# Performance work log

Measured on AMD Instinct MI355X. Metric: run time of the kernel, lower is better.

## Reference

```python
import jax, jax.numpy as jnp
import numpy as np

N = 100000   # nodes
E = 1600000  # edges
C = 128      # hidden_channels
L = 3        # num_layers
V = 128      # embedding vocab


def setup_inputs() -> dict:
    key = jax.random.key(0)
    ks = jax.random.split(key, 10)
    s = 1.0 / np.sqrt(C)
    return {
        "x_idx": jax.random.randint(ks[0], (N,), 0, V),
        "edge_index": jax.random.randint(ks[1], (2, E), 0, N),
        "edge_weight": jax.random.uniform(ks[2], (E,), dtype=jnp.float32),
        "emb": jax.random.normal(ks[3], (V, C), dtype=jnp.float32),
        "conv_w": jax.random.uniform(ks[4], (L, C, C), minval=-s, maxval=s, dtype=jnp.float32),
        "conv_b": jnp.zeros((L, C), dtype=jnp.float32),
        "lin1_w": jax.random.uniform(ks[5], (C, C), minval=-s, maxval=s, dtype=jnp.float32),
        "lin1_b": jnp.zeros((C,), dtype=jnp.float32),
        "lin2_w": jax.random.uniform(ks[6], (C, 2), minval=-s, maxval=s, dtype=jnp.float32),
        "lin2_b": jnp.zeros((2,), dtype=jnp.float32),
    }


def reference(x_idx, edge_index, edge_weight, emb, conv_w, conv_b,
              lin1_w, lin1_b, lin2_w, lin2_b):
    # GCNConv (PyG): add self-loops (weight 1), symmetric normalization
    row, col = edge_index[0], edge_index[1]
    loop = jnp.arange(N)
    r = jnp.concatenate([row, loop])
    c = jnp.concatenate([col, loop])
    w = jnp.concatenate([edge_weight, jnp.ones((N,), edge_weight.dtype)])
    deg = jax.ops.segment_sum(w, c, num_segments=N)            # [N]
    dinv = jnp.where(deg > 0, jax.lax.rsqrt(deg), 0.0)
    norm = dinv[r] * w * dinv[c]                               # [E+N]

    x = emb[x_idx]                                             # [N, C]
    for i in range(L):
        xw = x @ conv_w[i]                                     # [N, C]
        # message: norm * xw[src], aggregate at dst
        x = jax.ops.segment_sum(norm[:, None] * xw[r], c, num_segments=N) + conv_b[i]
        if i < L - 1:
            x = jax.nn.relu(x)  # dropout is identity in eval mode

    x = jax.nn.relu(x @ lin1_w + lin1_b)
    return x @ lin2_w + lin2_b                                 # [N, 2]
```

## Files before the change

### kernel.cpp

```cpp
#include <hip/hip_runtime.h>
#include <hip/hip_fp16.h>

#define NN 100000
#define NE 1600000
#define CC 128
#define NB_SCAN 391

typedef _Float16 f16x8 __attribute__((ext_vector_type(8)));
typedef float    f32x4 __attribute__((ext_vector_type(4)));

__global__ void k_init(int* cnt) {
    int i = blockIdx.x * 256 + threadIdx.x;
    if (i < NN) cnt[i] = 0;
}

__global__ void k_count(const int* __restrict__ ei, int* cnt, int* loc) {
    int e = blockIdx.x * 256 + threadIdx.x;
    if (e < NE) {
        int c = ei[NE + e];
        loc[e] = atomicAdd(&cnt[c], 1);
    }
}

__global__ void k_scan1(const int* __restrict__ cnt, int* rowptr, int* bsum) {
    __shared__ int s[256];
    int t = threadIdx.x;
    int i = blockIdx.x * 256 + t;
    int v = (i < NN) ? cnt[i] : 0;
    s[t] = v; __syncthreads();
    for (int off = 1; off < 256; off <<= 1) {
        int x = (t >= off) ? s[t - off] : 0;
        __syncthreads();
        s[t] += x;
        __syncthreads();
    }
    if (i < NN) rowptr[i] = s[t] - v;
    if (t == 255) bsum[blockIdx.x] = s[255];
}

__global__ void k_scan2(const int* __restrict__ bsum, int* boff) {
    __shared__ int s[512];
    int t = threadIdx.x;
    int v = (t < NB_SCAN) ? bsum[t] : 0;
    s[t] = v; __syncthreads();
    for (int off = 1; off < 512; off <<= 1) {
        int x = (t >= off) ? s[t - off] : 0;
        __syncthreads();
        s[t] += x;
        __syncthreads();
    }
    if (t < NB_SCAN) boff[t] = s[t] - v;
}

__global__ void k_scan3(int* rowptr, const int* __restrict__ boff) {
    int i = blockIdx.x * 256 + threadIdx.x;
    if (i < NN) rowptr[i] += boff[i >> 8];
    if (i == 0) rowptr[NN] = NE;
}

__global__ void k_scatter(const int* __restrict__ ei, const float* __restrict__ ew,
                          const int* __restrict__ loc, const int* __restrict__ rowptr,
                          int2* __restrict__ csr) {
    int e = blockIdx.x * 256 + threadIdx.x;
    if (e < NE) {
        int c = ei[NE + e];
        int pos = rowptr[c] + loc[e];
        csr[pos] = make_int2(ei[e], __float_as_int(ew[e]));
    }
}

__global__ void k_degdinv(const int* __restrict__ rowptr, const int2* __restrict__ csr,
                          float* __restrict__ dinv) {
    int v = blockIdx.x * 256 + threadIdx.x;
    if (v < NN) {
        int b = rowptr[v], e = rowptr[v + 1];
        float s = 1.f;
        for (int i = b; i < e; i++) s += __int_as_float(csr[i].y);
        dinv[v] = rsqrtf(s);
    }
}

__global__ void k_mkcsr0(const int2* __restrict__ csr, const int* __restrict__ xidx,
                         const float* __restrict__ dinv, int2* __restrict__ csr0) {
    int e = blockIdx.x * 256 + threadIdx.x;
    if (e < NE) {
        int2 c = csr[e];
        csr0[e] = make_int2(xidx[c.x],
                            __float_as_int(__int_as_float(c.y) * dinv[c.x]));
    }
}

__global__ void k_wcvt(const float* __restrict__ conv_w, const float* __restrict__ lin1_w,
                       _Float16* __restrict__ wt) {
    int t = blockIdx.x * 256 + threadIdx.x;
    int l = t >> 14, r = t & 16383;
    int j = r >> 7, k = r & 127;
    const float* src = (l < 2) ? (conv_w + (l + 1) * 16384) : lin1_w;
    wt[l * 16384 + j * 128 + k] = (_Float16)src[k * 128 + j];
}

__global__ void k_embw(const float* __restrict__ emb, const float* __restrict__ w0,
                       __half2* __restrict__ ewh) {
    int t = blockIdx.x * 256 + threadIdx.x;
    int i = t >> 6, jp = t & 63;
    int j0 = jp * 2;
    float a0 = 0.f, a1 = 0.f;
    for (int k = 0; k < 128; k++) {
        float e = emb[i * 128 + k];
        a0 = fmaf(e, w0[k * 128 + j0], a0);
        a1 = fmaf(e, w0[k * 128 + j0 + 1], a1);
    }
    ewh[t] = __floats2half2_rn(a0, a1);
}

__global__ void k_agg0(const int2* __restrict__ csr0, const int* __restrict__ rowptr,
                       const int* __restrict__ xidx, const float* __restrict__ dinv,
                       const __half2* __restrict__ ewh, const float* __restrict__ bias,
                       __half2* __restrict__ xout) {
    int wave = threadIdx.x >> 6, lane = threadIdx.x & 63;
    int v = blockIdx.x * 4 + wave;
    if (v >= NN) return;
    int beg = rowptr[v], end = rowptr[v + 1];
    float ax = 0.f, ay = 0.f;
    int e = beg;
    while (e + 8 <= end) {
        int2 c[8]; __half2 t[8];
#pragma unroll
        for (int u = 0; u < 8; u++) c[u] = csr0[e + u];
#pragma unroll
        for (int u = 0; u < 8; u++) t[u] = ewh[c[u].x * 64 + lane];
#pragma unroll
        for (int u = 0; u < 8; u++) {
            float w = __int_as_float(c[u].y);
            float2 f = __half22float2(t[u]);
            ax = fmaf(w, f.x, ax);
            ay = fmaf(w, f.y, ay);
        }
        e += 8;
    }
    if (e + 4 <= end) {
        int2 c[4]; __half2 t[4];
#pragma unroll
        for (int u = 0; u < 4; u++) c[u] = csr0[e + u];
#pragma unroll
        for (int u = 0; u < 4; u++) t[u] = ewh[c[u].x * 64 + lane];
#pragma unroll
        for (int u = 0; u < 4; u++) {
            float w = __int_as_float(c[u].y);
            float2 f = __half22float2(t[u]);
            ax = fmaf(w, f.x, ax);
            ay = fmaf(w, f.y, ay);
        }
        e += 4;
    }
    for (; e < end; ++e) {
        int2 c = csr0[e];
        float w = __int_as_float(c.y);
        float2 f = __half22float2(ewh[c.x * 64 + lane]);
        ax = fmaf(w, f.x, ax);
        ay = fmaf(w, f.y, ay);
    }
    float dv = dinv[v];
    float2 ts = __half22float2(ewh[xidx[v] * 64 + lane]);
    ax = fmaf(dv, ts.x, ax);
    ay = fmaf(dv, ts.y, ay);
    float2 b = reinterpret_cast<const float2*>(bias)[lane];
    float ox = fmaxf(fmaf(dv, ax, b.x), 0.f);
    float oy = fmaxf(fmaf(dv, ay, b.y), 0.f);
    xout[v * 64 + lane] = __floats2half2_rn(ox, oy);
}

__global__ void k_agg(const __half2* __restrict__ y2, const int* __restrict__ rowptr,
                      const int2* __restrict__ csr, const float* __restrict__ dinv,
                      const float* __restrict__ bias, __half2* __restrict__ xout,
                      int relu) {
    int wave = threadIdx.x >> 6, lane = threadIdx.x & 63;
    int v = blockIdx.x * 4 + wave;
    if (v >= NN) return;
    int beg = rowptr[v], end = rowptr[v + 1];
    float ax = 0.f, ay = 0.f;
    int e = beg;
    while (e + 8 <= end) {
        int2 c[8]; __half2 t[8];
#pragma unroll
        for (int u = 0; u < 8; u++) c[u] = csr[e + u];
#pragma unroll
        for (int u = 0; u < 8; u++) t[u] = y2[c[u].x * 64 + lane];
#pragma unroll
        for (int u = 0; u < 8; u++) {
            float w = __int_as_float(c[u].y);
            float2 f = __half22float2(t[u]);
            ax = fmaf(w, f.x, ax);
            ay = fmaf(w, f.y, ay);
        }
        e += 8;
    }
    if (e + 4 <= end) {
        int2 c[4]; __half2 t[4];
#pragma unroll
        for (int u = 0; u < 4; u++) c[u] = csr[e + u];
#pragma unroll
        for (int u = 0; u < 4; u++) t[u] = y2[c[u].x * 64 + lane];
#pragma unroll
        for (int u = 0; u < 4; u++) {
            float w = __int_as_float(c[u].y);
            float2 f = __half22float2(t[u]);
            ax = fmaf(w, f.x, ax);
            ay = fmaf(w, f.y, ay);
        }
        e += 4;
    }
    for (; e < end; ++e) {
        int2 c = csr[e];
        float w = __int_as_float(c.y);
        float2 f = __half22float2(y2[c.x * 64 + lane]);
        ax = fmaf(w, f.x, ax);
        ay = fmaf(w, f.y, ay);
    }
    float2 self = __half22float2(y2[v * 64 + lane]);
    ax += self.x; ay += self.y;
    float s = dinv[v];
    float2 b = reinterpret_cast<const float2*>(bias)[lane];
    float ox = fmaf(s, ax, b.x);
    float oy = fmaf(s, ay, b.y);
    if (relu) { ox = fmaxf(ox, 0.f); oy = fmaxf(oy, 0.f); }
    xout[v * 64 + lane] = __floats2half2_rn(ox, oy);
}

template <int MODE>
__global__ __launch_bounds__(256) void k_mgemm(const _Float16* __restrict__ A,
                                               const _Float16* __restrict__ Wt,
                                               const float* __restrict__ dinv,
                                               const float* __restrict__ bias,
                                               _Float16* __restrict__ yout,
                                               const float* __restrict__ w2,
                                               const float* __restrict__ b2,
                                               float* __restrict__ outf) {
    int wid = threadIdx.x >> 6, lane = threadIdx.x & 63;
    int lc = lane & 15, lg = lane >> 4;
    int arow = blockIdx.x * 64 + wid * 16 + lc;
    bool rok = arow < NN;

    f32x4 acc[8];
#pragma unroll
    for (int j = 0; j < 8; j++) acc[j] = (f32x4){0.f, 0.f, 0.f, 0.f};

#pragma unroll
    for (int kc = 0; kc < 4; kc++) {
        int k0 = kc * 32 + lg * 8;
        f16x8 a = {0, 0, 0, 0, 0, 0, 0, 0};
        if (rok) a = *reinterpret_cast<const f16x8*>(&A[arow * 128 + k0]);
#pragma unroll
        for (int j = 0; j < 8; j++) {
            f16x8 b = *reinterpret_cast<const f16x8*>(&Wt[(j * 16 + lc) * 128 + k0]);
            acc[j] = __builtin_amdgcn_mfma_f32_16x16x32_f16(a, b, acc[j], 0, 0, 0);
        }
    }

    int orow0 = blockIdx.x * 64 + wid * 16 + lg * 4;
    if (MODE == 0) {
        float dv[4];
#pragma unroll
        for (int r = 0; r < 4; r++)
            dv[r] = (orow0 + r < NN) ? dinv[orow0 + r] : 0.f;
#pragma unroll
        for (int j = 0; j < 8; j++) {
#pragma unroll
            for (int r = 0; r < 4; r++) {
                int orow = orow0 + r;
                if (orow < NN)
                    yout[orow * 128 + j * 16 + lc] = (_Float16)(dv[r] * acc[j][r]);
            }
        }
    } else {
        float bj[8], w0j[8], w1j[8];
#pragma unroll
        for (int j = 0; j < 8; j++) {
            int c = j * 16 + lc;
            bj[j] = bias[c];
            w0j[j] = w2[c * 2 + 0];
            w1j[j] = w2[c * 2 + 1];
        }
        float bb0 = b2[0], bb1 = b2[1];
#pragma unroll
        for (int r = 0; r < 4; r++) {
            float p0 = 0.f, p1 = 0.f;
#pragma unroll
            for (int j = 0; j < 8; j++) {
                float h = fmaxf(acc[j][r] + bj[j], 0.f);
                p0 = fmaf(h, w0j[j], p0);
                p1 = fmaf(h, w1j[j], p1);
            }
#pragma unroll
            for (int m = 1; m < 16; m <<= 1) {
                p0 += __shfl_xor(p0, m);
                p1 += __shfl_xor(p1, m);
            }
            int orow = orow0 + r;
            if (lc == 0 && orow < NN)
                *reinterpret_cast<float2*>(&outf[orow * 2]) =
                    make_float2(p0 + bb0, p1 + bb1);
        }
    }
}

extern "C" void kernel_launch(void* const* d_in, const int* in_sizes, int n_in,
                              void* d_out, int out_size, void* d_ws, size_t ws_size,
                              hipStream_t stream) {
    const int*   x_idx  = (const int*)d_in[0];
    const int*   ei     = (const int*)d_in[1];
    const float* ew     = (const float*)d_in[2];
    const float* emb    = (const float*)d_in[3];
    const float* conv_w = (const float*)d_in[4];
    const float* conv_b = (const float*)d_in[5];
    const float* lin1_w = (const float*)d_in[6];
    const float* lin1_b = (const float*)d_in[7];
    const float* lin2_w = (const float*)d_in[8];
    const float* lin2_b = (const float*)d_in[9];
    float* out = (float*)d_out;

    char* ws = (char*)d_ws;
    size_t off = 0;
    auto alloc = [&](size_t bytes) -> void* {
        void* p = ws + off;
        off += (bytes + 255) & ~(size_t)255;
        return p;
    };
    float*    dinv   = (float*)alloc(NN * 4);
    int*      cnt    = (int*)alloc(NN * 4);
    int*      rowptr = (int*)alloc((NN + 1) * 4);
    int*      bsum   = (int*)alloc(512 * 4);
    int*      boff   = (int*)alloc(512 * 4);
    int*      loc    = (int*)alloc((size_t)NE * 4);
    int2*     csr    = (int2*)alloc((size_t)NE * 8);
    int2*     csr0   = (int2*)alloc((size_t)NE * 8);
    __half2*  ewh    = (__half2*)alloc(128 * 64 * 4);
    _Float16* wt     = (_Float16*)alloc(3 * 128 * 128 * 2);
    __half*   xbuf   = (__half*)alloc((size_t)NN * CC * 2);
    __half*   ybuf   = (__half*)alloc((size_t)NN * CC * 2);
    (void)ws_size;

    const int NBn = (NN + 255) / 256;
    const int NBe = (NE + 255) / 256;
    const int NBg = (NN + 63) / 64;

    k_init<<<NBn, 256, 0, stream>>>(cnt);
    k_count<<<NBe, 256, 0, stream>>>(ei, cnt, loc);
    k_scan1<<<NB_SCAN, 256, 0, stream>>>(cnt, rowptr, bsum);
    k_scan2<<<1, 512, 0, stream>>>(bsum, boff);
    k_scan3<<<NBn, 256, 0, stream>>>(rowptr, boff);
    k_scatter<<<NBe, 256, 0, stream>>>(ei, ew, loc, rowptr, csr);
    k_degdinv<<<NBn, 256, 0, stream>>>(rowptr, csr, dinv);
    k_mkcsr0<<<NBe, 256, 0, stream>>>(csr, x_idx, dinv, csr0);
    k_wcvt<<<192, 256, 0, stream>>>(conv_w, lin1_w, wt);

    k_embw<<<32, 256, 0, stream>>>(emb, conv_w, ewh);
    k_agg0<<<NN / 4, 256, 0, stream>>>(csr0, rowptr, x_idx, dinv, ewh,
                                       conv_b + 0 * CC, (__half2*)xbuf);
    k_mgemm<0><<<NBg, 256, 0, stream>>>((const _Float16*)xbuf, wt + 0 * 16384, dinv,
                                        nullptr, (_Float16*)ybuf, nullptr, nullptr,
                                        nullptr);
    k_agg<<<NN / 4, 256, 0, stream>>>((const __half2*)ybuf, rowptr, csr, dinv,
                                      conv_b + 1 * CC, (__half2*)xbuf, 1);
    k_mgemm<0><<<NBg, 256, 0, stream>>>((const _Float16*)xbuf, wt + 1 * 16384, dinv,
                                        nullptr, (_Float16*)ybuf, nullptr, nullptr,
                                        nullptr);
    k_agg<<<NN / 4, 256, 0, stream>>>((const __half2*)ybuf, rowptr, csr, dinv,
                                      conv_b + 2 * CC, (__half2*)xbuf, 0);
    k_mgemm<1><<<NBg, 256, 0, stream>>>((const _Float16*)xbuf, wt + 2 * 16384, dinv,
                                        lin1_b, nullptr, lin2_w, lin2_b, out);
}
```

Baseline: 444.6 us.

## Pad CSR rows to multiples of 4 and gather 4 edges per wave

Each node's CSR segment is padded to a multiple of 4 edges, with zero-weight padding entries that come from a memset of a larger buffer. The aggregation kernels split each wave into 4 groups of 16 lanes, so one wave loads 4 neighbor rows at a time with 16-byte f16x8 loads, then combines the partial sums with cross-lane shuffles. The intent is wider, fewer memory transactions and no tail loops, at the cost of a memset, larger CSR buffers, extra padding work and shuffle reductions.

```diff
diff --git a/kernel.cpp b/kernel.cpp
--- a/kernel.cpp
+++ b/kernel.cpp
@@ -5,6 +5,7 @@
 #define NE 1600000
 #define CC 128
 #define NB_SCAN 391
+#define CAP 1900032
 
 typedef _Float16 f16x8 __attribute__((ext_vector_type(8)));
 typedef float    f32x4 __attribute__((ext_vector_type(4)));
@@ -26,7 +27,7 @@
     __shared__ int s[256];
     int t = threadIdx.x;
     int i = blockIdx.x * 256 + t;
-    int v = (i < NN) ? cnt[i] : 0;
+    int v = (i < NN) ? ((cnt[i] + 3) & ~3) : 0;
     s[t] = v; __syncthreads();
     for (int off = 1; off < 256; off <<= 1) {
         int x = (t >= off) ? s[t - off] : 0;
@@ -52,10 +53,13 @@
     if (t < NB_SCAN) boff[t] = s[t] - v;
 }
 
-__global__ void k_scan3(int* rowptr, const int* __restrict__ boff) {
+__global__ void k_scan3(int* rowptr, const int* __restrict__ boff,
+                        const int* __restrict__ cnt) {
     int i = blockIdx.x * 256 + threadIdx.x;
-    if (i < NN) rowptr[i] += boff[i >> 8];
-    if (i == 0) rowptr[NN] = NE;
+    if (i < NN) {
+        rowptr[i] += boff[i >> 8];
+        if (i == NN - 1) rowptr[NN] = rowptr[i] + ((cnt[i] + 3) & ~3);
+    }
 }
 
 __global__ void k_scatter(const int* __restrict__ ei, const float* __restrict__ ew,
@@ -83,7 +87,7 @@
 __global__ void k_mkcsr0(const int2* __restrict__ csr, const int* __restrict__ xidx,
                          const float* __restrict__ dinv, int2* __restrict__ csr0) {
     int e = blockIdx.x * 256 + threadIdx.x;
-    if (e < NE) {
+    if (e < CAP) {
         int2 c = csr[e];
         csr0[e] = make_int2(xidx[c.x],
                             __float_as_int(__int_as_float(c.y) * dinv[c.x]));
@@ -113,118 +117,83 @@
     ewh[t] = __floats2half2_rn(a0, a1);
 }
 
-__global__ void k_agg0(const int2* __restrict__ csr0, const int* __restrict__ rowptr,
-                       const int* __restrict__ xidx, const float* __restrict__ dinv,
-                       const __half2* __restrict__ ewh, const float* __restrict__ bias,
-                       __half2* __restrict__ xout) {
+template <int SELF_TABLE, int RELU>
+__device__ __forceinline__ void agg_core(const _Float16* __restrict__ src16,
+                                         const int2* __restrict__ csr,
+                                         const int* __restrict__ rowptr,
+                                         const int* __restrict__ xidx,
+                                         const float* __restrict__ dinv,
+                                         const float* __restrict__ bias,
+                                         _Float16* __restrict__ xout) {
     int wave = threadIdx.x >> 6, lane = threadIdx.x & 63;
+    int g = lane >> 4, sub = lane & 15;
     int v = blockIdx.x * 4 + wave;
     if (v >= NN) return;
     int beg = rowptr[v], end = rowptr[v + 1];
-    float ax = 0.f, ay = 0.f;
+    float acc[8];
+#pragma unroll
+    for (int i = 0; i < 8; i++) acc[i] = 0.f;
     int e = beg;
     while (e + 8 <= end) {
-        int2 c[8]; __half2 t[8];
-#pragma unroll
-        for (int u = 0; u < 8; u++) c[u] = csr0[e + u];
-#pragma unroll
-        for (int u = 0; u < 8; u++) t[u] = ewh[c[u].x * 64 + lane];
-#pragma unroll
-        for (int u = 0; u < 8; u++) {
-            float w = __int_as_float(c[u].y);
-            float2 f = __half22float2(t[u]);
-            ax = fmaf(w, f.x, ax);
-            ay = fmaf(w, f.y, ay);
-        }
+        int2 c0 = csr[e + g];
+        int2 c1 = csr[e + 4 + g];
+        f16x8 t0 = *reinterpret_cast<const f16x8*>(&src16[(size_t)c0.x * 128 + sub * 8]);
+        f16x8 t1 = *reinterpret_cast<const f16x8*>(&src16[(size_t)c1.x * 128 + sub * 8]);
+        float w0 = __int_as_float(c0.y), w1 = __int_as_float(c1.y);
+#pragma unroll
+        for (int i = 0; i < 8; i++) acc[i] = fmaf(w0, (float)t0[i], acc[i]);
+#pragma unroll
+        for (int i = 0; i < 8; i++) acc[i] = fmaf(w1, (float)t1[i], acc[i]);
         e += 8;
     }
-    if (e + 4 <= end) {
-        int2 c[4]; __half2 t[4];
-#pragma unroll
-        for (int u = 0; u < 4; u++) c[u] = csr0[e + u];
-#pragma unroll
-        for (int u = 0; u < 4; u++) t[u] = ewh[c[u].x * 64 + lane];
-#pragma unroll
-        for (int u = 0; u < 4; u++) {
-            float w = __int_as_float(c[u].y);
-            float2 f = __half22float2(t[u]);
-            ax = fmaf(w, f.x, ax);
-            ay = fmaf(w, f.y, ay);
-        }
-        e += 4;
-    }
-    for (; e < end; ++e) {
-        int2 c = csr0[e];
-        float w = __int_as_float(c.y);
-        float2 f = __half22float2(ewh[c.x * 64 + lane]);
-        ax = fmaf(w, f.x, ax);
-        ay = fmaf(w, f.y, ay);
-    }
-    float dv = dinv[v];
-    float2 ts = __half22float2(ewh[xidx[v] * 64 + lane]);
-    ax = fmaf(dv, ts.x, ax);
-    ay = fmaf(dv, ts.y, ay);
-    float2 b = reinterpret_cast<const float2*>(bias)[lane];
-    float ox = fmaxf(fmaf(dv, ax, b.x), 0.f);
-    float oy = fmaxf(fmaf(dv, ay, b.y), 0.f);
-    xout[v * 64 + lane] = __floats2half2_rn(ox, oy);
-}
-
-__global__ void k_agg(const __half2* __restrict__ y2, const int* __restrict__ rowptr,
-                      const int2* __restrict__ csr, const float* __restrict__ dinv,
-                      const float* __restrict__ bias, __half2* __restrict__ xout,
-                      int relu) {
-    int wave = threadIdx.x >> 6, lane = threadIdx.x & 63;
-    int v = blockIdx.x * 4 + wave;
-    if (v >= NN) return;
-    int beg = rowptr[v], end = rowptr[v + 1];
-    float ax = 0.f, ay = 0.f;
-    int e = beg;
-    while (e + 8 <= end) {
-        int2 c[8]; __half2 t[8];
-#pragma unroll
-        for (int u = 0; u < 8; u++) c[u] = csr[e + u];
-#pragma unroll
-        for (int u = 0; u < 8; u++) t[u] = y2[c[u].x * 64 + lane];
-#pragma unroll
-        for (int u = 0; u < 8; u++) {
-            float w = __int_as_float(c[u].y);
-            float2 f = __half22float2(t[u]);
-            ax = fmaf(w, f.x, ax);
-            ay = fmaf(w, f.y, ay);
-        }
-        e += 8;
-    }
-    if (e + 4 <= end) {
-        int2 c[4]; __half2 t[4];
-#pragma unroll
-        for (int u = 0; u < 4; u++) c[u] = csr[e + u];
-#pragma unroll
-        for (int u = 0; u < 4; u++) t[u] = y2[c[u].x * 64 + lane];
-#pragma unroll
-        for (int u = 0; u < 4; u++) {
-            float w = __int_as_float(c[u].y);
-            float2 f = __half22float2(t[u]);
-            ax = fmaf(w, f.x, ax);
-            ay = fmaf(w, f.y, ay);
-        }
-        e += 4;
-    }
-    for (; e < end; ++e) {
-        int2 c = csr[e];
-        float w = __int_as_float(c.y);
-        float2 f = __half22float2(y2[c.x * 64 + lane]);
-        ax = fmaf(w, f.x, ax);
-        ay = fmaf(w, f.y, ay);
-    }
-    float2 self = __half22float2(y2[v * 64 + lane]);
-    ax += self.x; ay += self.y;
-    float s = dinv[v];
-    float2 b = reinterpret_cast<const float2*>(bias)[lane];
-    float ox = fmaf(s, ax, b.x);
-    float oy = fmaf(s, ay, b.y);
-    if (relu) { ox = fmaxf(ox, 0.f); oy = fmaxf(oy, 0.f); }
-    xout[v * 64 + lane] = __floats2half2_rn(ox, oy);
+    if (e < end) {
+        int2 c0 = csr[e + g];
+        f16x8 t0 = *reinterpret_cast<const f16x8*>(&src16[(size_t)c0.x * 128 + sub * 8]);
+        float w0 = __int_as_float(c0.y);
+#pragma unroll
+        for (int i = 0; i < 8; i++) acc[i] = fmaf(w0, (float)t0[i], acc[i]);
+    }
+#pragma unroll
+    for (int i = 0; i < 8; i++) {
+        acc[i] += __shfl_down(acc[i], 32);
+        acc[i] += __shfl_down(acc[i], 16);
+    }
+    if (g == 0) {
+        float dv = dinv[v];
+        size_t selfoff = SELF_TABLE ? (size_t)xidx[v] * 128 : (size_t)v * 128;
+        f16x8 sf = *reinterpret_cast<const f16x8*>(&src16[selfoff + sub * 8]);
+        float4 b0 = reinterpret_cast<const float4*>(bias)[sub * 2];
+        float4 b1 = reinterpret_cast<const float4*>(bias)[sub * 2 + 1];
+        float bb[8] = {b0.x, b0.y, b0.z, b0.w, b1.x, b1.y, b1.z, b1.w};
+        f16x8 o;
+#pragma unroll
+        for (int i = 0; i < 8; i++) {
+            float self = SELF_TABLE ? dv * (float)sf[i] : (float)sf[i];
+            float r = fmaf(dv, acc[i] + self, bb[i]);
+            if (RELU) r = fmaxf(r, 0.f);
+            o[i] = (_Float16)r;
+        }
+        *reinterpret_cast<f16x8*>(&xout[(size_t)v * 128 + sub * 8]) = o;
+    }
+}
+
+__global__ void k_agg0(const int2* __restrict__ csr0, const int* __restrict__ rowptr,
+                       const int* __restrict__ xidx, const float* __restrict__ dinv,
+                       const _Float16* __restrict__ ewh, const float* __restrict__ bias,
+                       _Float16* __restrict__ xout) {
+    agg_core<1, 1>(ewh, csr0, rowptr, xidx, dinv, bias, xout);
+}
+
+__global__ void k_agg_r(const _Float16* __restrict__ y, const int* __restrict__ rowptr,
+                        const int2* __restrict__ csr, const float* __restrict__ dinv,
+                        const float* __restrict__ bias, _Float16* __restrict__ xout) {
+    agg_core<0, 1>(y, csr, rowptr, nullptr, dinv, bias, xout);
+}
+
+__global__ void k_agg_n(const _Float16* __restrict__ y, const int* __restrict__ rowptr,
+                        const int2* __restrict__ csr, const float* __restrict__ dinv,
+                        const float* __restrict__ bias, _Float16* __restrict__ xout) {
+    agg_core<0, 0>(y, csr, rowptr, nullptr, dinv, bias, xout);
 }
 
 template <int MODE>
@@ -332,41 +301,39 @@
     int*      bsum   = (int*)alloc(512 * 4);
     int*      boff   = (int*)alloc(512 * 4);
     int*      loc    = (int*)alloc((size_t)NE * 4);
-    int2*     csr    = (int2*)alloc((size_t)NE * 8);
-    int2*     csr0   = (int2*)alloc((size_t)NE * 8);
-    __half2*  ewh    = (__half2*)alloc(128 * 64 * 4);
+    int2*     csr    = (int2*)alloc((size_t)CAP * 8);
+    int2*     csr0   = (int2*)alloc((size_t)CAP * 8);
+    _Float16* ewh    = (_Float16*)alloc(128 * 128 * 2);
     _Float16* wt     = (_Float16*)alloc(3 * 128 * 128 * 2);
-    __half*   xbuf   = (__half*)alloc((size_t)NN * CC * 2);
-    __half*   ybuf   = (__half*)alloc((size_t)NN * CC * 2);
+    _Float16* xbuf   = (_Float16*)alloc((size_t)NN * CC * 2);
+    _Float16* ybuf   = (_Float16*)alloc((size_t)NN * CC * 2);
     (void)ws_size;
 
     const int NBn = (NN + 255) / 256;
     const int NBe = (NE + 255) / 256;
+    const int NBc = CAP / 256;
     const int NBg = (NN + 63) / 64;
 
+    hipMemsetAsync(csr, 0, (size_t)CAP * 8, stream);
     k_init<<<NBn, 256, 0, stream>>>(cnt);
     k_count<<<NBe, 256, 0, stream>>>(ei, cnt, loc);
     k_scan1<<<NB_SCAN, 256, 0, stream>>>(cnt, rowptr, bsum);
     k_scan2<<<1, 512, 0, stream>>>(bsum, boff);
-    k_scan3<<<NBn, 256, 0, stream>>>(rowptr, boff);
+    k_scan3<<<NBn, 256, 0, stream>>>(rowptr, boff, cnt);
     k_scatter<<<NBe, 256, 0, stream>>>(ei, ew, loc, rowptr, csr);
     k_degdinv<<<NBn, 256, 0, stream>>>(rowptr, csr, dinv);
-    k_mkcsr0<<<NBe, 256, 0, stream>>>(csr, x_idx, dinv, csr0);
+    k_mkcsr0<<<NBc, 256, 0, stream>>>(csr, x_idx, dinv, csr0);
     k_wcvt<<<192, 256, 0, stream>>>(conv_w, lin1_w, wt);
 
-    k_embw<<<32, 256, 0, stream>>>(emb, conv_w, ewh);
+    k_embw<<<32, 256, 0, stream>>>(emb, conv_w, (__half2*)ewh);
     k_agg0<<<NN / 4, 256, 0, stream>>>(csr0, rowptr, x_idx, dinv, ewh,
-                                       conv_b + 0 * CC, (__half2*)xbuf);
-    k_mgemm<0><<<NBg, 256, 0, stream>>>((const _Float16*)xbuf, wt + 0 * 16384, dinv,
-                                        nullptr, (_Float16*)ybuf, nullptr, nullptr,
-                                        nullptr);
-    k_agg<<<NN / 4, 256, 0, stream>>>((const __half2*)ybuf, rowptr, csr, dinv,
-                                      conv_b + 1 * CC, (__half2*)xbuf, 1);
-    k_mgemm<0><<<NBg, 256, 0, stream>>>((const _Float16*)xbuf, wt + 1 * 16384, dinv,
-                                        nullptr, (_Float16*)ybuf, nullptr, nullptr,
-                                        nullptr);
-    k_agg<<<NN / 4, 256, 0, stream>>>((const __half2*)ybuf, rowptr, csr, dinv,
-                                      conv_b + 2 * CC, (__half2*)xbuf, 0);
-    k_mgemm<1><<<NBg, 256, 0, stream>>>((const _Float16*)xbuf, wt + 2 * 16384, dinv,
-                                        lin1_b, nullptr, lin2_w, lin2_b, out);
-}
+                                       conv_b + 0 * CC, xbuf);
+    k_mgemm<0><<<NBg, 256, 0, stream>>>(xbuf, wt + 0 * 16384, dinv, nullptr, ybuf,
+                                        nullptr, nullptr, nullptr);
+    k_agg_r<<<NN / 4, 256, 0, stream>>>(ybuf, rowptr, csr, dinv, conv_b + 1 * CC, xbuf);
+    k_mgemm<0><<<NBg, 256, 0, stream>>>(xbuf, wt + 1 * 16384, dinv, nullptr, ybuf,
+                                        nullptr, nullptr, nullptr);
+    k_agg_n<<<NN / 4, 256, 0, stream>>>(ybuf, rowptr, csr, dinv, conv_b + 2 * CC, xbuf);
+    k_mgemm<1><<<NBg, 256, 0, stream>>>(xbuf, wt + 2 * 16384, dinv, lin1_b, nullptr,
+                                        lin2_w, lin2_b, out);
+}
```

New measurement: 432.9 us. -2.6%, faster.
